# Kernel tuning notes

Hardware: AMD Instinct MI355X
Metric: run time of the kernel (lower is better)

Reference implementation:

```python
import jax, jax.numpy as jnp
import numpy as np

N_NODES = 50000


def _add_self_loops(edge_index, num_nodes):
    loops = jnp.arange(num_nodes, dtype=edge_index.dtype)
    src = jnp.concatenate([edge_index[0], loops])
    dst = jnp.concatenate([edge_index[1], loops])
    return src, dst


def _gcn_conv(x, src, dst, W, b, num_nodes):
    # Linear transform first (smaller of the two dims is typical, matches PyG)
    h = x @ W  # [N, out]
    # Symmetric normalization with unit edge weights (self-loops included)
    deg = jax.ops.segment_sum(jnp.ones_like(dst, dtype=h.dtype), dst, num_segments=num_nodes)
    dinv = jnp.where(deg > 0, jax.lax.rsqrt(deg), 0.0)
    norm = dinv[src] * dinv[dst]  # [E]
    msg = h[src] * norm[:, None]  # gather + scale
    out = jax.ops.segment_sum(msg, dst, num_segments=num_nodes)  # scatter-add
    return out + b


def setup_inputs() -> dict:
    key = jax.random.key(0)
    k1, k2, k3, k4, k5, k6 = jax.random.split(key, 6)
    in_dim, hid, half = 128, 128, 64
    x = jax.random.normal(k1, (N_NODES, in_dim), dtype=jnp.float32)
    edge_index = jax.random.randint(k2, (2, 800000), 0, N_NODES, dtype=jnp.int32)
    # Glorot-style init for GCN weights, zero bias (PyG default)
    W1 = jax.random.normal(k3, (in_dim, hid), dtype=jnp.float32) * (1.0 / np.sqrt(in_dim))
    b1 = jnp.zeros((hid,), dtype=jnp.float32)
    W2 = jax.random.normal(k4, (hid, half), dtype=jnp.float32) * (1.0 / np.sqrt(hid))
    b2 = jnp.zeros((half,), dtype=jnp.float32)
    return {"x": x, "edge_index": edge_index, "W1": W1, "b1": b1, "W2": W2, "b2": b2}


def reference(x, edge_index, W1, b1, W2, b2):
    src, dst = _add_self_loops(edge_index, N_NODES)
    h = jax.nn.relu(_gcn_conv(x, src, dst, W1, b1, N_NODES))
    h = jax.nn.relu(_gcn_conv(h, src, dst, W2, b2, N_NODES))
    return h
```

## Files before the change

kernel.cpp:

```cpp
#include <hip/hip_runtime.h>

#define NN 50000
#define NE 800000
#define NBUCK 196
#define BCAP 5120
#define NPART 256
#define EPP (NE / NPART)

typedef short short8 __attribute__((ext_vector_type(8)));
typedef float f32x4 __attribute__((ext_vector_type(4)));
union U4 { uint4 u; short8 h; };

__device__ __forceinline__ unsigned f2bf(float f) {
  union { float f; unsigned u; } v; v.f = f;
  return (v.u + 0x7FFFu + ((v.u >> 16) & 1u)) >> 16;
}
__device__ __forceinline__ float2 upk(unsigned u) {
  union { unsigned u; float f; } a, b;
  a.u = u << 16; b.u = u & 0xFFFF0000u;
  return make_float2(a.f, b.f);
}
__device__ __forceinline__ float bf2f(unsigned short b) {
  union { unsigned u; float f; } v; v.u = ((unsigned)b) << 16;
  return v.f;
}
__device__ __forceinline__ unsigned pk2(float a, float b) {
  return f2bf(a) | (f2bf(b) << 16);
}

__global__ __launch_bounds__(256) void k_prep(const float* __restrict__ W1,
                                              const float* __restrict__ W2,
                                              unsigned short* __restrict__ W1T,
                                              unsigned short* __restrict__ W2T,
                                              unsigned* __restrict__ gcur) {
  int b = blockIdx.x, t = threadIdx.x;
  if (b == 0 && t < NBUCK) gcur[t] = 0;
  {
    int idx = b * 256 + t;
    int k = idx >> 7, n = idx & 127;
    W1T[(n << 7) + (k ^ ((n & 7) << 3))] = (unsigned short)f2bf(W1[idx]);
  }
  {
    if (t < 128) {
      int idx = b * 128 + t;
      int k = idx >> 6, n = idx & 63;
      W2T[(n << 7) + (k ^ ((n & 7) << 3))] = (unsigned short)f2bf(W2[idx]);
    }
  }
}

__global__ __launch_bounds__(256) void k_partmm1(const int* __restrict__ src,
                                                 const int* __restrict__ dst,
                                                 unsigned* __restrict__ gcur,
                                                 unsigned* __restrict__ part,
                                                 const float* __restrict__ X,
                                                 const unsigned short* __restrict__ W1T,
                                                 unsigned* __restrict__ Hbu) {
  __shared__ __attribute__((aligned(16))) unsigned smem[12288];
  __shared__ int wsum[4];
  const int tid = threadIdx.x;
  if (blockIdx.x < NPART) {
    unsigned* stage = smem;
    unsigned* hist  = smem + 3200;
    unsigned* curs  = smem + 3400;
    unsigned* bbs   = smem + 3600;
    const int e0 = blockIdx.x * EPP;
    for (int i = tid; i < NBUCK; i += 256) hist[i] = 0;
    __syncthreads();
    for (int k = tid; k < EPP; k += 256)
      atomicAdd(&hist[((unsigned)dst[e0 + k]) >> 8], 1u);
    __syncthreads();
    {
      int lane = tid & 63, w = tid >> 6;
      unsigned v = (tid < NBUCK) ? hist[tid] : 0;
      unsigned incl = v;
#pragma unroll
      for (int d = 1; d < 64; d <<= 1) {
        unsigned u = __shfl_up(incl, d);
        if (lane >= d) incl += u;
      }
      if (lane == 63) wsum[w] = (int)incl;
      __syncthreads();
      unsigned wpre = 0;
      for (int j = 0; j < w; ++j) wpre += (unsigned)wsum[j];
      if (tid < NBUCK) curs[tid] = wpre + incl - v;
    }
    __syncthreads();
    for (int k = tid; k < EPP; k += 256) {
      int d = dst[e0 + k];
      unsigned slot = atomicAdd(&curs[((unsigned)d) >> 8], 1u);
      stage[slot] = (((unsigned)src[e0 + k]) << 16) | (unsigned)d;
    }
    __syncthreads();
    if (tid < NBUCK) bbs[tid] = atomicAdd(&gcur[tid], hist[tid]);
    __syncthreads();
    for (int k = tid; k < EPP; k += 256) {
      unsigned v = stage[k];
      unsigned b = (v & 0xFFFFu) >> 8;
      unsigned startb = curs[b] - hist[b];
      part[b * BCAP + bbs[b] + ((unsigned)k - startb)] = v;
    }
  } else {
    uint4* w1t4 = (uint4*)smem;
    uint4* xs4  = (uint4*)(smem + 8192);
    const int base = (blockIdx.x - NPART) * 64;
    const uint4* W1Tg = (const uint4*)W1T;
    const float4* X4 = (const float4*)X;
#pragma unroll
    for (int it = 0; it < 8; ++it) w1t4[tid + 256 * it] = W1Tg[tid + 256 * it];
#pragma unroll
    for (int it = 0; it < 4; ++it) {
      int j = tid + 256 * it;
      int row = j >> 4, c16 = j & 15;
      int grow = base + row;
      uint4 v = make_uint4(0, 0, 0, 0);
      if (grow < NN) {
        float4 f0 = X4[(size_t)grow * 32 + c16 * 2];
        float4 f1 = X4[(size_t)grow * 32 + c16 * 2 + 1];
        v = make_uint4(pk2(f0.x, f0.y), pk2(f0.z, f0.w), pk2(f1.x, f1.y), pk2(f1.z, f1.w));
      }
      xs4[row * 16 + (c16 ^ (row & 7))] = v;
    }
    __syncthreads();
    const int lane = tid & 63, wv = tid >> 6;
    const int l7 = lane & 7, lg = lane >> 4;
    f32x4 acc[8];
#pragma unroll
    for (int c = 0; c < 8; ++c) acc[c] = (f32x4){0.f, 0.f, 0.f, 0.f};
    const int arow = wv * 16 + (lane & 15);
#pragma unroll
    for (int kk = 0; kk < 4; ++kk) {
      int kcc = kk * 4 + lg;
      U4 a; a.u = xs4[arow * 16 + (kcc ^ l7)];
#pragma unroll
      for (int c = 0; c < 8; ++c) {
        int n = c * 16 + (lane & 15);
        U4 b; b.u = w1t4[n * 16 + (kcc ^ l7)];
        acc[c] = __builtin_amdgcn_mfma_f32_16x16x32_bf16(a.h, b.h, acc[c], 0, 0, 0);
      }
    }
#pragma unroll
    for (int c = 0; c < 8; ++c) {
#pragma unroll
      for (int r = 0; r < 4; ++r) {
        int grow = base + wv * 16 + lg * 4 + r;
        unsigned mb = f2bf(acc[c][r]);
        unsigned ob = (unsigned)__shfl_xor((int)mb, 1);
        if (((lane & 1) == 0) && grow < NN)
          Hbu[(size_t)grow * 64 + c * 8 + ((lane & 15) >> 1)] = mb | (ob << 16);
      }
    }
  }
}

__global__ void k_bksc(const unsigned* __restrict__ gcur, unsigned* __restrict__ bbase) {
  __shared__ int wsum[4];
  int tid = threadIdx.x;
  int lane = tid & 63, w = tid >> 6;
  unsigned v = (tid < NBUCK) ? gcur[tid] : 0;
  unsigned incl = v;
#pragma unroll
  for (int d = 1; d < 64; d <<= 1) {
    unsigned u = __shfl_up(incl, d);
    if (lane >= d) incl += u;
  }
  if (lane == 63) wsum[w] = (int)incl;
  __syncthreads();
  unsigned wpre = 0;
  for (int j = 0; j < w; ++j) wpre += (unsigned)wsum[j];
  if (tid < NBUCK) bbase[tid] = wpre + incl - v;
}

__global__ __launch_bounds__(256) void k_bucket(const unsigned* __restrict__ gcur,
                                                const unsigned* __restrict__ bbase,
                                                const unsigned* __restrict__ part,
                                                int* __restrict__ off,
                                                float* __restrict__ dinv,
                                                unsigned short* __restrict__ ssrc) {
  __shared__ unsigned hist[256], curs[256];
  __shared__ unsigned short ssr[BCAP];
  __shared__ int wsum[4];
  const int tid = threadIdx.x, b = blockIdx.x;
  const int nb = (int)gcur[b];
  const int base = (int)bbase[b];
  const unsigned* pp = part + (size_t)b * BCAP;
  hist[tid] = 0;
  __syncthreads();
  for (int k = tid; k < nb; k += 256) atomicAdd(&hist[pp[k] & 255u], 1u);
  __syncthreads();
  unsigned v = hist[tid];
  int lane = tid & 63, w = tid >> 6;
  unsigned incl = v;
#pragma unroll
  for (int d = 1; d < 64; d <<= 1) {
    unsigned u = __shfl_up(incl, d);
    if (lane >= d) incl += u;
  }
  if (lane == 63) wsum[w] = (int)incl;
  __syncthreads();
  unsigned wpre = 0;
  for (int j = 0; j < w; ++j) wpre += (unsigned)wsum[j];
  unsigned excl = wpre + incl - v;
  curs[tid] = excl;
  int node = b * 256 + tid;
  if (node < NN) {
    off[node] = base + (int)excl;
    dinv[node] = rsqrtf((float)(v + 1));
  } else if (node == NN) {
    off[NN] = base + (int)excl;
  }
  __syncthreads();
  for (int k = tid; k < nb; k += 256) {
    unsigned vv = pp[k];
    unsigned slot = atomicAdd(&curs[vv & 255u], 1u);
    ssr[slot] = (unsigned short)(vv >> 16);
  }
  __syncthreads();
  for (int k = tid; k < nb; k += 256) ssrc[base + k] = ssr[k];
}

__global__ __launch_bounds__(256) void k_agg1(const unsigned* __restrict__ Hb,
                                              const int* __restrict__ off,
                                              const unsigned short* __restrict__ ssrc,
                                              const float* __restrict__ dinv,
                                              const float* __restrict__ b1,
                                              unsigned* __restrict__ H2) {
  int n = (blockIdx.x * 256 + threadIdx.x) >> 6;
  int lane = threadIdx.x & 63;
  if (n >= NN) return;
  float dn = dinv[n];
  int jb = off[n], je = off[n + 1];
  float2 self = upk(Hb[(size_t)n * 64 + lane]);
  float2 acc = make_float2(dn * self.x, dn * self.y);
  int j = jb;
  for (; j + 7 < je; j += 8) {
    int s0 = ssrc[j], s1 = ssrc[j + 1], s2 = ssrc[j + 2], s3 = ssrc[j + 3];
    int s4 = ssrc[j + 4], s5 = ssrc[j + 5], s6 = ssrc[j + 6], s7 = ssrc[j + 7];
    float w0 = dinv[s0], w1 = dinv[s1], w2 = dinv[s2], w3 = dinv[s3];
    float w4 = dinv[s4], w5 = dinv[s5], w6 = dinv[s6], w7 = dinv[s7];
    unsigned u0 = Hb[(size_t)s0 * 64 + lane], u1 = Hb[(size_t)s1 * 64 + lane];
    unsigned u2 = Hb[(size_t)s2 * 64 + lane], u3 = Hb[(size_t)s3 * 64 + lane];
    unsigned u4 = Hb[(size_t)s4 * 64 + lane], u5 = Hb[(size_t)s5 * 64 + lane];
    unsigned u6 = Hb[(size_t)s6 * 64 + lane], u7 = Hb[(size_t)s7 * 64 + lane];
    float2 f0 = upk(u0), f1 = upk(u1), f2 = upk(u2), f3 = upk(u3);
    float2 f4 = upk(u4), f5 = upk(u5), f6 = upk(u6), f7 = upk(u7);
    acc.x = fmaf(f0.x, w0, acc.x); acc.y = fmaf(f0.y, w0, acc.y);
    acc.x = fmaf(f1.x, w1, acc.x); acc.y = fmaf(f1.y, w1, acc.y);
    acc.x = fmaf(f2.x, w2, acc.x); acc.y = fmaf(f2.y, w2, acc.y);
    acc.x = fmaf(f3.x, w3, acc.x); acc.y = fmaf(f3.y, w3, acc.y);
    acc.x = fmaf(f4.x, w4, acc.x); acc.y = fmaf(f4.y, w4, acc.y);
    acc.x = fmaf(f5.x, w5, acc.x); acc.y = fmaf(f5.y, w5, acc.y);
    acc.x = fmaf(f6.x, w6, acc.x); acc.y = fmaf(f6.y, w6, acc.y);
    acc.x = fmaf(f7.x, w7, acc.x); acc.y = fmaf(f7.y, w7, acc.y);
  }
  for (; j < je; ++j) {
    int s0 = ssrc[j];
    float w0 = dinv[s0];
    float2 f = upk(Hb[(size_t)s0 * 64 + lane]);
    acc.x = fmaf(f.x, w0, acc.x);
    acc.y = fmaf(f.y, w0, acc.y);
  }
  float2 b = ((const float2*)b1)[lane];
  float hx = fmaxf(fmaf(dn, acc.x, b.x), 0.f);
  float hy = fmaxf(fmaf(dn, acc.y, b.y), 0.f);
  H2[(size_t)n * 64 + lane] = pk2(hx, hy);
}

__global__ __launch_bounds__(256) void k_mm2(const unsigned* __restrict__ H2,
                                             const unsigned short* __restrict__ W2T,
                                             const float* __restrict__ dinv,
                                             unsigned* __restrict__ H3u) {
  __shared__ __attribute__((aligned(16))) unsigned smem[8192];
  uint4* w2t4 = (uint4*)smem;
  uint4* xs4  = (uint4*)(smem + 4096);
  const int tid = threadIdx.x;
  const int base = blockIdx.x * 64;
  const uint4* W2Tg = (const uint4*)W2T;
  const uint4* H2v = (const uint4*)H2;
#pragma unroll
  for (int it = 0; it < 4; ++it) w2t4[tid + 256 * it] = W2Tg[tid + 256 * it];
#pragma unroll
  for (int it = 0; it < 4; ++it) {
    int j = tid + 256 * it;
    int row = j >> 4, c16 = j & 15;
    int grow = base + row;
    uint4 v = (grow < NN) ? H2v[(size_t)grow * 16 + c16] : make_uint4(0, 0, 0, 0);
    xs4[row * 16 + (c16 ^ (row & 7))] = v;
  }
  __syncthreads();
  const int lane = tid & 63, wv = tid >> 6;
  const int l7 = lane & 7, lg = lane >> 4;
  f32x4 acc[4];
#pragma unroll
  for (int c = 0; c < 4; ++c) acc[c] = (f32x4){0.f, 0.f, 0.f, 0.f};
  const int arow = wv * 16 + (lane & 15);
#pragma unroll
  for (int kk = 0; kk < 4; ++kk) {
    int kcc = kk * 4 + lg;
    U4 a; a.u = xs4[arow * 16 + (kcc ^ l7)];
#pragma unroll
    for (int c = 0; c < 4; ++c) {
      int n = c * 16 + (lane & 15);
      U4 b; b.u = w2t4[n * 16 + (kcc ^ l7)];
      acc[c] = __builtin_amdgcn_mfma_f32_16x16x32_bf16(a.h, b.h, acc[c], 0, 0, 0);
    }
  }
#pragma unroll
  for (int c = 0; c < 4; ++c) {
#pragma unroll
    for (int r = 0; r < 4; ++r) {
      int grow = base + wv * 16 + lg * 4 + r;
      float dn = (grow < NN) ? dinv[grow] : 0.f;
      unsigned mb = f2bf(acc[c][r] * dn);
      unsigned ob = (unsigned)__shfl_xor((int)mb, 1);
      if (((lane & 1) == 0) && grow < NN)
        H3u[(size_t)grow * 32 + c * 8 + ((lane & 15) >> 1)] = mb | (ob << 16);
    }
  }
}

__global__ __launch_bounds__(256) void k_agg2(const unsigned short* __restrict__ H3,
                                              const int* __restrict__ off,
                                              const unsigned short* __restrict__ ssrc,
                                              const float* __restrict__ dinv,
                                              const float* __restrict__ b2,
                                              float* __restrict__ out) {
  int n = (blockIdx.x * 256 + threadIdx.x) >> 6;
  int lane = threadIdx.x & 63;
  if (n >= NN) return;
  float dn = dinv[n];
  int jb = off[n], je = off[n + 1];
  float acc = bf2f(H3[(size_t)n * 64 + lane]);
  int j = jb;
  for (; j + 7 < je; j += 8) {
    int s0 = ssrc[j], s1 = ssrc[j + 1], s2 = ssrc[j + 2], s3 = ssrc[j + 3];
    int s4 = ssrc[j + 4], s5 = ssrc[j + 5], s6 = ssrc[j + 6], s7 = ssrc[j + 7];
    float h0 = bf2f(H3[(size_t)s0 * 64 + lane]);
    float h1 = bf2f(H3[(size_t)s1 * 64 + lane]);
    float h2 = bf2f(H3[(size_t)s2 * 64 + lane]);
    float h3 = bf2f(H3[(size_t)s3 * 64 + lane]);
    float h4 = bf2f(H3[(size_t)s4 * 64 + lane]);
    float h5 = bf2f(H3[(size_t)s5 * 64 + lane]);
    float h6 = bf2f(H3[(size_t)s6 * 64 + lane]);
    float h7 = bf2f(H3[(size_t)s7 * 64 + lane]);
    acc += h0 + h1 + h2 + h3 + h4 + h5 + h6 + h7;
  }
  for (; j < je; ++j) acc += bf2f(H3[(size_t)ssrc[j] * 64 + lane]);
  out[(size_t)n * 64 + lane] = fmaxf(fmaf(dn, acc, b2[lane]), 0.f);
}

extern "C" void kernel_launch(void* const* d_in, const int* in_sizes, int n_in,
                              void* d_out, int out_size, void* d_ws, size_t ws_size,
                              hipStream_t stream) {
  const float* x  = (const float*)d_in[0];
  const int*   ei = (const int*)d_in[1];
  const float* W1 = (const float*)d_in[2];
  const float* b1 = (const float*)d_in[3];
  const float* W2 = (const float*)d_in[4];
  const float* b2 = (const float*)d_in[5];
  const int* esrc = ei;
  const int* edst = ei + NE;

  char* ws = (char*)d_ws;
  unsigned* gcur  = (unsigned*)(ws + 0);
  unsigned* bbase = (unsigned*)(ws + 1024);
  int*      off   = (int*)(ws + 2048);
  float*    dinv  = (float*)(ws + 204800);
  unsigned short* ssrc = (unsigned short*)(ws + 405504);
  unsigned short* W1T  = (unsigned short*)(ws + 2013184);
  unsigned short* W2T  = (unsigned short*)(ws + 2045952);
  unsigned* part  = (unsigned*)(ws + 2097152);
  unsigned* Hb    = (unsigned*)(ws + 6291456);
  unsigned* H2    = (unsigned*)(ws + 19922944);
  unsigned short* H3 = (unsigned short*)(ws + 33554432);

  hipLaunchKernelGGL(k_prep, dim3(64), dim3(256), 0, stream, W1, W2, W1T, W2T, gcur);
  hipLaunchKernelGGL(k_partmm1, dim3(NPART + (NN + 63) / 64), dim3(256), 0, stream,
                     esrc, edst, gcur, part, x, W1T, Hb);
  hipLaunchKernelGGL(k_bksc, dim3(1), dim3(256), 0, stream, gcur, bbase);
  hipLaunchKernelGGL(k_bucket, dim3(NBUCK), dim3(256), 0, stream,
                     gcur, bbase, part, off, dinv, ssrc);
  hipLaunchKernelGGL(k_agg1, dim3((NN + 3) / 4), dim3(256), 0, stream,
                     Hb, off, ssrc, dinv, b1, H2);
  hipLaunchKernelGGL(k_mm2, dim3((NN + 63) / 64), dim3(256), 0, stream,
                     H2, W2T, dinv, (unsigned*)H3);
  hipLaunchKernelGGL(k_agg2, dim3((NN + 3) / 4), dim3(256), 0, stream,
                     H3, off, ssrc, dinv, b2, (float*)d_out);
}
```

Before: 120.6 us.

## Fold bucket scan into k_bucket, prescale Hb by dinv, vectorize index loads

Removes the single-block bucket-scan kernel by having every k_bucket block recompute the 196-entry prefix scan redundantly. k_bucket also rescales its 256 rows of Hb by the source-side dinv in place, so k_agg1 can do plain adds without gathering dinv per edge. Both aggregation kernels align the edge range to 8 and load eight 16-bit source indices with one 128-bit load. The trade-off is an extra read-modify-write pass over Hb in k_bucket, plus a second bf16 rounding of the prescaled features.

New measurement: 145.8 us. 20.8% more time.

```diff
diff --git a/kernel.cpp b/kernel.cpp
--- a/kernel.cpp
+++ b/kernel.cpp
@@ -153,43 +153,41 @@
   }
 }
 
-__global__ void k_bksc(const unsigned* __restrict__ gcur, unsigned* __restrict__ bbase) {
-  __shared__ int wsum[4];
-  int tid = threadIdx.x;
-  int lane = tid & 63, w = tid >> 6;
-  unsigned v = (tid < NBUCK) ? gcur[tid] : 0;
-  unsigned incl = v;
-#pragma unroll
-  for (int d = 1; d < 64; d <<= 1) {
-    unsigned u = __shfl_up(incl, d);
-    if (lane >= d) incl += u;
-  }
-  if (lane == 63) wsum[w] = (int)incl;
-  __syncthreads();
-  unsigned wpre = 0;
-  for (int j = 0; j < w; ++j) wpre += (unsigned)wsum[j];
-  if (tid < NBUCK) bbase[tid] = wpre + incl - v;
-}
-
 __global__ __launch_bounds__(256) void k_bucket(const unsigned* __restrict__ gcur,
-                                                const unsigned* __restrict__ bbase,
                                                 const unsigned* __restrict__ part,
                                                 int* __restrict__ off,
                                                 float* __restrict__ dinv,
-                                                unsigned short* __restrict__ ssrc) {
-  __shared__ unsigned hist[256], curs[256];
+                                                unsigned short* __restrict__ ssrc,
+                                                unsigned* __restrict__ Hb) {
+  __shared__ unsigned hist[256], curs[256], sb[256];
+  __shared__ float dvs[256];
   __shared__ unsigned short ssr[BCAP];
   __shared__ int wsum[4];
   const int tid = threadIdx.x, b = blockIdx.x;
+  const int lane = tid & 63, w = tid >> 6;
+  {
+    unsigned g = (tid < NBUCK) ? gcur[tid] : 0;
+    unsigned incl = g;
+#pragma unroll
+    for (int d = 1; d < 64; d <<= 1) {
+      unsigned u = __shfl_up(incl, d);
+      if (lane >= d) incl += u;
+    }
+    if (lane == 63) wsum[w] = (int)incl;
+    __syncthreads();
+    unsigned wpre = 0;
+    for (int j = 0; j < w; ++j) wpre += (unsigned)wsum[j];
+    sb[tid] = wpre + incl - g;
+  }
+  __syncthreads();
   const int nb = (int)gcur[b];
-  const int base = (int)bbase[b];
+  const int base = (int)sb[b];
   const unsigned* pp = part + (size_t)b * BCAP;
   hist[tid] = 0;
   __syncthreads();
   for (int k = tid; k < nb; k += 256) atomicAdd(&hist[pp[k] & 255u], 1u);
   __syncthreads();
   unsigned v = hist[tid];
-  int lane = tid & 63, w = tid >> 6;
   unsigned incl = v;
 #pragma unroll
   for (int d = 1; d < 64; d <<= 1) {
@@ -202,10 +200,12 @@
   for (int j = 0; j < w; ++j) wpre += (unsigned)wsum[j];
   unsigned excl = wpre + incl - v;
   curs[tid] = excl;
+  float dv = rsqrtf((float)(v + 1));
+  dvs[tid] = dv;
   int node = b * 256 + tid;
   if (node < NN) {
     off[node] = base + (int)excl;
-    dinv[node] = rsqrtf((float)(v + 1));
+    dinv[node] = dv;
   } else if (node == NN) {
     off[NN] = base + (int)excl;
   }
@@ -217,6 +217,23 @@
   }
   __syncthreads();
   for (int k = tid; k < nb; k += 256) ssrc[base + k] = ssr[k];
+  uint4* HbT = (uint4*)Hb + (size_t)b * 4096;
+#pragma unroll
+  for (int i = 0; i < 16; ++i) {
+    int idx = tid + 256 * i;
+    int row = idx >> 4;
+    int grow = b * 256 + row;
+    if (grow < NN) {
+      uint4 u = HbT[idx];
+      float s = dvs[row];
+      float2 a0 = upk(u.x), a1 = upk(u.y), a2 = upk(u.z), a3 = upk(u.w);
+      u.x = pk2(a0.x * s, a0.y * s);
+      u.y = pk2(a1.x * s, a1.y * s);
+      u.z = pk2(a2.x * s, a2.y * s);
+      u.w = pk2(a3.x * s, a3.y * s);
+      HbT[idx] = u;
+    }
+  }
 }
 
 __global__ __launch_bounds__(256) void k_agg1(const unsigned* __restrict__ Hb,
@@ -230,35 +247,32 @@
   if (n >= NN) return;
   float dn = dinv[n];
   int jb = off[n], je = off[n + 1];
-  float2 self = upk(Hb[(size_t)n * 64 + lane]);
-  float2 acc = make_float2(dn * self.x, dn * self.y);
+  float2 acc = upk(Hb[(size_t)n * 64 + lane]);
   int j = jb;
+  int ja = (jb + 7) & ~7;
+  if (ja > je) ja = je;
+  for (; j < ja; ++j) {
+    float2 f = upk(Hb[(size_t)ssrc[j] * 64 + lane]);
+    acc.x += f.x; acc.y += f.y;
+  }
   for (; j + 7 < je; j += 8) {
-    int s0 = ssrc[j], s1 = ssrc[j + 1], s2 = ssrc[j + 2], s3 = ssrc[j + 3];
-    int s4 = ssrc[j + 4], s5 = ssrc[j + 5], s6 = ssrc[j + 6], s7 = ssrc[j + 7];
-    float w0 = dinv[s0], w1 = dinv[s1], w2 = dinv[s2], w3 = dinv[s3];
-    float w4 = dinv[s4], w5 = dinv[s5], w6 = dinv[s6], w7 = dinv[s7];
+    uint4 sp = *(const uint4*)(ssrc + j);
+    unsigned s0 = sp.x & 0xFFFFu, s1 = sp.x >> 16;
+    unsigned s2 = sp.y & 0xFFFFu, s3 = sp.y >> 16;
+    unsigned s4 = sp.z & 0xFFFFu, s5 = sp.z >> 16;
+    unsigned s6 = sp.w & 0xFFFFu, s7 = sp.w >> 16;
     unsigned u0 = Hb[(size_t)s0 * 64 + lane], u1 = Hb[(size_t)s1 * 64 + lane];
     unsigned u2 = Hb[(size_t)s2 * 64 + lane], u3 = Hb[(size_t)s3 * 64 + lane];
     unsigned u4 = Hb[(size_t)s4 * 64 + lane], u5 = Hb[(size_t)s5 * 64 + lane];
     unsigned u6 = Hb[(size_t)s6 * 64 + lane], u7 = Hb[(size_t)s7 * 64 + lane];
     float2 f0 = upk(u0), f1 = upk(u1), f2 = upk(u2), f3 = upk(u3);
     float2 f4 = upk(u4), f5 = upk(u5), f6 = upk(u6), f7 = upk(u7);
-    acc.x = fmaf(f0.x, w0, acc.x); acc.y = fmaf(f0.y, w0, acc.y);
-    acc.x = fmaf(f1.x, w1, acc.x); acc.y = fmaf(f1.y, w1, acc.y);
-    acc.x = fmaf(f2.x, w2, acc.x); acc.y = fmaf(f2.y, w2, acc.y);
-    acc.x = fmaf(f3.x, w3, acc.x); acc.y = fmaf(f3.y, w3, acc.y);
-    acc.x = fmaf(f4.x, w4, acc.x); acc.y = fmaf(f4.y, w4, acc.y);
-    acc.x = fmaf(f5.x, w5, acc.x); acc.y = fmaf(f5.y, w5, acc.y);
-    acc.x = fmaf(f6.x, w6, acc.x); acc.y = fmaf(f6.y, w6, acc.y);
-    acc.x = fmaf(f7.x, w7, acc.x); acc.y = fmaf(f7.y, w7, acc.y);
+    acc.x += f0.x + f1.x + f2.x + f3.x + f4.x + f5.x + f6.x + f7.x;
+    acc.y += f0.y + f1.y + f2.y + f3.y + f4.y + f5.y + f6.y + f7.y;
   }
   for (; j < je; ++j) {
-    int s0 = ssrc[j];
-    float w0 = dinv[s0];
-    float2 f = upk(Hb[(size_t)s0 * 64 + lane]);
-    acc.x = fmaf(f.x, w0, acc.x);
-    acc.y = fmaf(f.y, w0, acc.y);
+    float2 f = upk(Hb[(size_t)ssrc[j] * 64 + lane]);
+    acc.x += f.x; acc.y += f.y;
   }
   float2 b = ((const float2*)b1)[lane];
   float hx = fmaxf(fmaf(dn, acc.x, b.x), 0.f);
@@ -332,9 +346,15 @@
   int jb = off[n], je = off[n + 1];
   float acc = bf2f(H3[(size_t)n * 64 + lane]);
   int j = jb;
+  int ja = (jb + 7) & ~7;
+  if (ja > je) ja = je;
+  for (; j < ja; ++j) acc += bf2f(H3[(size_t)ssrc[j] * 64 + lane]);
   for (; j + 7 < je; j += 8) {
-    int s0 = ssrc[j], s1 = ssrc[j + 1], s2 = ssrc[j + 2], s3 = ssrc[j + 3];
-    int s4 = ssrc[j + 4], s5 = ssrc[j + 5], s6 = ssrc[j + 6], s7 = ssrc[j + 7];
+    uint4 sp = *(const uint4*)(ssrc + j);
+    unsigned s0 = sp.x & 0xFFFFu, s1 = sp.x >> 16;
+    unsigned s2 = sp.y & 0xFFFFu, s3 = sp.y >> 16;
+    unsigned s4 = sp.z & 0xFFFFu, s5 = sp.z >> 16;
+    unsigned s6 = sp.w & 0xFFFFu, s7 = sp.w >> 16;
     float h0 = bf2f(H3[(size_t)s0 * 64 + lane]);
     float h1 = bf2f(H3[(size_t)s1 * 64 + lane]);
     float h2 = bf2f(H3[(size_t)s2 * 64 + lane]);
@@ -363,7 +383,6 @@
 
   char* ws = (char*)d_ws;
   unsigned* gcur  = (unsigned*)(ws + 0);
-  unsigned* bbase = (unsigned*)(ws + 1024);
   int*      off   = (int*)(ws + 2048);
   float*    dinv  = (float*)(ws + 204800);
   unsigned short* ssrc = (unsigned short*)(ws + 405504);
@@ -377,9 +396,8 @@
   hipLaunchKernelGGL(k_prep, dim3(64), dim3(256), 0, stream, W1, W2, W1T, W2T, gcur);
   hipLaunchKernelGGL(k_partmm1, dim3(NPART + (NN + 63) / 64), dim3(256), 0, stream,
                      esrc, edst, gcur, part, x, W1T, Hb);
-  hipLaunchKernelGGL(k_bksc, dim3(1), dim3(256), 0, stream, gcur, bbase);
   hipLaunchKernelGGL(k_bucket, dim3(NBUCK), dim3(256), 0, stream,
-                     gcur, bbase, part, off, dinv, ssrc);
+                     gcur, part, off, dinv, ssrc, Hb);
   hipLaunchKernelGGL(k_agg1, dim3((NN + 3) / 4), dim3(256), 0, stream,
                      Hb, off, ssrc, dinv, b1, H2);
   hipLaunchKernelGGL(k_mm2, dim3((NN + 63) / 64), dim3(256), 0, stream,
```

## Precompute degree normalization early, fold source dinv into H, restructure layer-1 aggregation

Applied to the files above, without the earlier changes.

Adds separate degree-histogram and merge kernels so dinv exists before the first matmul, which then pre-scales each H row by its source dinv. That lets layer-1 aggregation drop the per-edge dinv gather and just sum neighbor rows. The aggregation is reorganized so 16-lane groups handle 16-column slices over a grid-strided tile loop. The bucket-offset scan is folded into k_bucket, removing one launch. This adds two small kernels and reads dst one more time, and reuses the H2 buffer region for partial histograms.

Measured after the change: 171.6 us. 42.3% more time.

```diff
diff --git a/kernel.cpp b/kernel.cpp
--- a/kernel.cpp
+++ b/kernel.cpp
@@ -26,6 +26,41 @@
 }
 __device__ __forceinline__ unsigned pk2(float a, float b) {
   return f2bf(a) | (f2bf(b) << 16);
+}
+
+__global__ __launch_bounds__(256) void k_deg_hist(const int* __restrict__ dst,
+                                                  unsigned* __restrict__ partial) {
+  __shared__ unsigned h[12500];
+  const int b = blockIdx.x, tid = threadIdx.x;
+  const int e0 = b * 12500;
+  unsigned* pb = partial + (size_t)b * 25000;
+#pragma unroll
+  for (int r = 0; r < 2; ++r) {
+    for (int i = tid; i < 12500; i += 256) h[i] = 0;
+    __syncthreads();
+    const int lo = r * 25000;
+    for (int k = tid; k < 12500; k += 256) {
+      int ld = dst[e0 + k] - lo;
+      if ((unsigned)ld < 25000u)
+        atomicAdd(&h[ld >> 1], 1u << (16 * (ld & 1)));
+    }
+    __syncthreads();
+    for (int i = tid; i < 12500; i += 256) pb[r * 12500 + i] = h[i];
+    __syncthreads();
+  }
+}
+
+__global__ __launch_bounds__(256) void k_deg_merge(const unsigned* __restrict__ partial,
+                                                   float* __restrict__ dinv) {
+  int w = blockIdx.x * 256 + threadIdx.x;
+  if (w >= 25000) return;
+  unsigned s0 = 0, s1 = 0;
+  for (int b = 0; b < 64; ++b) {
+    unsigned v = partial[(size_t)b * 25000 + w];
+    s0 += v & 0xFFFFu;
+    s1 += v >> 16;
+  }
+  ((float2*)dinv)[w] = make_float2(rsqrtf((float)(s0 + 1)), rsqrtf((float)(s1 + 1)));
 }
 
 __global__ __launch_bounds__(256) void k_prep(const float* __restrict__ W1,
@@ -40,12 +75,10 @@
     int k = idx >> 7, n = idx & 127;
     W1T[(n << 7) + (k ^ ((n & 7) << 3))] = (unsigned short)f2bf(W1[idx]);
   }
-  {
-    if (t < 128) {
-      int idx = b * 128 + t;
-      int k = idx >> 6, n = idx & 63;
-      W2T[(n << 7) + (k ^ ((n & 7) << 3))] = (unsigned short)f2bf(W2[idx]);
-    }
+  if (t < 128) {
+    int idx = b * 128 + t;
+    int k = idx >> 6, n = idx & 63;
+    W2T[(n << 7) + (k ^ ((n & 7) << 3))] = (unsigned short)f2bf(W2[idx]);
   }
 }
 
@@ -55,6 +88,7 @@
                                                  unsigned* __restrict__ part,
                                                  const float* __restrict__ X,
                                                  const unsigned short* __restrict__ W1T,
+                                                 const float* __restrict__ dinv,
                                                  unsigned* __restrict__ Hbu) {
   __shared__ __attribute__((aligned(16))) unsigned smem[12288];
   __shared__ int wsum[4];
@@ -144,7 +178,8 @@
 #pragma unroll
       for (int r = 0; r < 4; ++r) {
         int grow = base + wv * 16 + lg * 4 + r;
-        unsigned mb = f2bf(acc[c][r]);
+        float dn = (grow < NN) ? dinv[grow] : 0.f;
+        unsigned mb = f2bf(acc[c][r] * dn);
         unsigned ob = (unsigned)__shfl_xor((int)mb, 1);
         if (((lane & 1) == 0) && grow < NN)
           Hbu[(size_t)grow * 64 + c * 8 + ((lane & 15) >> 1)] = mb | (ob << 16);
@@ -153,43 +188,38 @@
   }
 }
 
-__global__ void k_bksc(const unsigned* __restrict__ gcur, unsigned* __restrict__ bbase) {
-  __shared__ int wsum[4];
-  int tid = threadIdx.x;
-  int lane = tid & 63, w = tid >> 6;
-  unsigned v = (tid < NBUCK) ? gcur[tid] : 0;
-  unsigned incl = v;
-#pragma unroll
-  for (int d = 1; d < 64; d <<= 1) {
-    unsigned u = __shfl_up(incl, d);
-    if (lane >= d) incl += u;
-  }
-  if (lane == 63) wsum[w] = (int)incl;
-  __syncthreads();
-  unsigned wpre = 0;
-  for (int j = 0; j < w; ++j) wpre += (unsigned)wsum[j];
-  if (tid < NBUCK) bbase[tid] = wpre + incl - v;
-}
-
 __global__ __launch_bounds__(256) void k_bucket(const unsigned* __restrict__ gcur,
-                                                const unsigned* __restrict__ bbase,
                                                 const unsigned* __restrict__ part,
                                                 int* __restrict__ off,
-                                                float* __restrict__ dinv,
                                                 unsigned short* __restrict__ ssrc) {
-  __shared__ unsigned hist[256], curs[256];
+  __shared__ unsigned hist[256], curs[256], sb[256];
   __shared__ unsigned short ssr[BCAP];
   __shared__ int wsum[4];
   const int tid = threadIdx.x, b = blockIdx.x;
+  const int lane = tid & 63, w = tid >> 6;
+  {
+    unsigned g = (tid < NBUCK) ? gcur[tid] : 0;
+    unsigned incl = g;
+#pragma unroll
+    for (int d = 1; d < 64; d <<= 1) {
+      unsigned u = __shfl_up(incl, d);
+      if (lane >= d) incl += u;
+    }
+    if (lane == 63) wsum[w] = (int)incl;
+    __syncthreads();
+    unsigned wpre = 0;
+    for (int j = 0; j < w; ++j) wpre += (unsigned)wsum[j];
+    sb[tid] = wpre + incl - g;
+  }
+  __syncthreads();
   const int nb = (int)gcur[b];
-  const int base = (int)bbase[b];
+  const int base = (int)sb[b];
   const unsigned* pp = part + (size_t)b * BCAP;
   hist[tid] = 0;
   __syncthreads();
   for (int k = tid; k < nb; k += 256) atomicAdd(&hist[pp[k] & 255u], 1u);
   __syncthreads();
   unsigned v = hist[tid];
-  int lane = tid & 63, w = tid >> 6;
   unsigned incl = v;
 #pragma unroll
   for (int d = 1; d < 64; d <<= 1) {
@@ -205,7 +235,6 @@
   int node = b * 256 + tid;
   if (node < NN) {
     off[node] = base + (int)excl;
-    dinv[node] = rsqrtf((float)(v + 1));
   } else if (node == NN) {
     off[NN] = base + (int)excl;
   }
@@ -225,45 +254,39 @@
                                               const float* __restrict__ dinv,
                                               const float* __restrict__ b1,
                                               unsigned* __restrict__ H2) {
-  int n = (blockIdx.x * 256 + threadIdx.x) >> 6;
-  int lane = threadIdx.x & 63;
-  if (n >= NN) return;
-  float dn = dinv[n];
-  int jb = off[n], je = off[n + 1];
-  float2 self = upk(Hb[(size_t)n * 64 + lane]);
-  float2 acc = make_float2(dn * self.x, dn * self.y);
-  int j = jb;
-  for (; j + 7 < je; j += 8) {
-    int s0 = ssrc[j], s1 = ssrc[j + 1], s2 = ssrc[j + 2], s3 = ssrc[j + 3];
-    int s4 = ssrc[j + 4], s5 = ssrc[j + 5], s6 = ssrc[j + 6], s7 = ssrc[j + 7];
-    float w0 = dinv[s0], w1 = dinv[s1], w2 = dinv[s2], w3 = dinv[s3];
-    float w4 = dinv[s4], w5 = dinv[s5], w6 = dinv[s6], w7 = dinv[s7];
-    unsigned u0 = Hb[(size_t)s0 * 64 + lane], u1 = Hb[(size_t)s1 * 64 + lane];
-    unsigned u2 = Hb[(size_t)s2 * 64 + lane], u3 = Hb[(size_t)s3 * 64 + lane];
-    unsigned u4 = Hb[(size_t)s4 * 64 + lane], u5 = Hb[(size_t)s5 * 64 + lane];
-    unsigned u6 = Hb[(size_t)s6 * 64 + lane], u7 = Hb[(size_t)s7 * 64 + lane];
-    float2 f0 = upk(u0), f1 = upk(u1), f2 = upk(u2), f3 = upk(u3);
-    float2 f4 = upk(u4), f5 = upk(u5), f6 = upk(u6), f7 = upk(u7);
-    acc.x = fmaf(f0.x, w0, acc.x); acc.y = fmaf(f0.y, w0, acc.y);
-    acc.x = fmaf(f1.x, w1, acc.x); acc.y = fmaf(f1.y, w1, acc.y);
-    acc.x = fmaf(f2.x, w2, acc.x); acc.y = fmaf(f2.y, w2, acc.y);
-    acc.x = fmaf(f3.x, w3, acc.x); acc.y = fmaf(f3.y, w3, acc.y);
-    acc.x = fmaf(f4.x, w4, acc.x); acc.y = fmaf(f4.y, w4, acc.y);
-    acc.x = fmaf(f5.x, w5, acc.x); acc.y = fmaf(f5.y, w5, acc.y);
-    acc.x = fmaf(f6.x, w6, acc.x); acc.y = fmaf(f6.y, w6, acc.y);
-    acc.x = fmaf(f7.x, w7, acc.x); acc.y = fmaf(f7.y, w7, acc.y);
-  }
-  for (; j < je; ++j) {
-    int s0 = ssrc[j];
-    float w0 = dinv[s0];
-    float2 f = upk(Hb[(size_t)s0 * 64 + lane]);
-    acc.x = fmaf(f.x, w0, acc.x);
-    acc.y = fmaf(f.y, w0, acc.y);
-  }
-  float2 b = ((const float2*)b1)[lane];
-  float hx = fmaxf(fmaf(dn, acc.x, b.x), 0.f);
-  float hy = fmaxf(fmaf(dn, acc.y, b.y), 0.f);
-  H2[(size_t)n * 64 + lane] = pk2(hx, hy);
+  const int tid = threadIdx.x;
+  const int lane = tid & 63, w = tid >> 6;
+  const int g = lane >> 4;
+  const int f = lane & 15;
+#pragma unroll
+  for (int p = 0; p < 4; ++p) {
+    const int col = p * 16 + f;
+    for (int tile = blockIdx.x; tile < NN / 16; tile += gridDim.x) {
+      const int n = tile * 16 + w * 4 + g;
+      int jb = off[n], je = off[n + 1];
+      float2 acc = upk(Hb[(size_t)n * 64 + col]);
+      int j = jb;
+      for (; j + 3 < je; j += 4) {
+        unsigned s0 = ssrc[j], s1 = ssrc[j + 1], s2 = ssrc[j + 2], s3 = ssrc[j + 3];
+        unsigned u0 = Hb[(size_t)s0 * 64 + col];
+        unsigned u1 = Hb[(size_t)s1 * 64 + col];
+        unsigned u2 = Hb[(size_t)s2 * 64 + col];
+        unsigned u3 = Hb[(size_t)s3 * 64 + col];
+        float2 f0 = upk(u0), f1 = upk(u1), f2 = upk(u2), f3 = upk(u3);
+        acc.x += f0.x + f1.x + f2.x + f3.x;
+        acc.y += f0.y + f1.y + f2.y + f3.y;
+      }
+      for (; j < je; ++j) {
+        float2 f0 = upk(Hb[(size_t)ssrc[j] * 64 + col]);
+        acc.x += f0.x;
+        acc.y += f0.y;
+      }
+      float dn = dinv[n];
+      float2 bb = ((const float2*)b1)[col];
+      H2[(size_t)n * 64 + col] = pk2(fmaxf(fmaf(dn, acc.x, bb.x), 0.f),
+                                     fmaxf(fmaf(dn, acc.y, bb.y), 0.f));
+    }
+  }
 }
 
 __global__ __launch_bounds__(256) void k_mm2(const unsigned* __restrict__ H2,
@@ -363,7 +386,6 @@
 
   char* ws = (char*)d_ws;
   unsigned* gcur  = (unsigned*)(ws + 0);
-  unsigned* bbase = (unsigned*)(ws + 1024);
   int*      off   = (int*)(ws + 2048);
   float*    dinv  = (float*)(ws + 204800);
   unsigned short* ssrc = (unsigned short*)(ws + 405504);
@@ -372,15 +394,17 @@
   unsigned* part  = (unsigned*)(ws + 2097152);
   unsigned* Hb    = (unsigned*)(ws + 6291456);
   unsigned* H2    = (unsigned*)(ws + 19922944);
+  unsigned* partial = (unsigned*)(ws + 19922944);
   unsigned short* H3 = (unsigned short*)(ws + 33554432);
 
+  hipLaunchKernelGGL(k_deg_hist, dim3(64), dim3(256), 0, stream, edst, partial);
   hipLaunchKernelGGL(k_prep, dim3(64), dim3(256), 0, stream, W1, W2, W1T, W2T, gcur);
+  hipLaunchKernelGGL(k_deg_merge, dim3(98), dim3(256), 0, stream, partial, dinv);
   hipLaunchKernelGGL(k_partmm1, dim3(NPART + (NN + 63) / 64), dim3(256), 0, stream,
-                     esrc, edst, gcur, part, x, W1T, Hb);
-  hipLaunchKernelGGL(k_bksc, dim3(1), dim3(256), 0, stream, gcur, bbase);
+                     esrc, edst, gcur, part, x, W1T, dinv, Hb);
   hipLaunchKernelGGL(k_bucket, dim3(NBUCK), dim3(256), 0, stream,
-                     gcur, bbase, part, off, dinv, ssrc);
-  hipLaunchKernelGGL(k_agg1, dim3((NN + 3) / 4), dim3(256), 0, stream,
+                     gcur, part, off, ssrc);
+  hipLaunchKernelGGL(k_agg1, dim3(2048), dim3(256), 0, stream,
                      Hb, off, ssrc, dinv, b1, H2);
   hipLaunchKernelGGL(k_mm2, dim3((NN + 63) / 64), dim3(256), 0, stream,
                      H2, W2T, dinv, (unsigned*)H3);
```
